# Performance work log

Measured on AMD Instinct MI355X. Metric: run time of the kernel, lower is better.

## Reference

```python
import jax, jax.numpy as jnp
import numpy as np
from jax import lax

S = 3000      # number of stocks (and number of targets)
F = 6         # raw features
N = 128       # hidden size
L = 40        # lookback length
L_MAX = 10    # max lag
K = 5         # topk leaders


def setup_inputs() -> dict:
    key = jax.random.key(0)
    ks = jax.random.split(key, 16)
    sc = 1.0 / np.sqrt(N)
    u = lambda k, shp, s=sc: jax.random.uniform(k, shp, jnp.float32, -s, s)
    return {
        "X_scaled": jax.random.normal(ks[0], (1, S, L, F), jnp.float32),
        "X_raw": jax.random.normal(ks[1], (1, S, L, F), jnp.float32),
        "target_idx": jax.random.randint(ks[2], (S,), 0, S, jnp.int32),
        "lstm_Wih": u(ks[3], (4 * N, F)),
        "lstm_Whh": u(ks[4], (4 * N, N)),
        "lstm_bih": u(ks[5], (4 * N,)),
        "lstm_bhh": u(ks[6], (4 * N,)),
        "ln_g": jnp.ones((N,), jnp.float32),
        "ln_b": jnp.zeros((N,), jnp.float32),
        "WQ": u(ks[7], (N, N)),
        "WK": u(ks[8], (N, N)),
        "log_temp": jnp.asarray(np.log(N ** 0.25), jnp.float32),
        "lag_bias": jnp.zeros((L_MAX,), jnp.float32),
        "W1": u(ks[9], (64, 2 * F), 1.0 / np.sqrt(2 * F)),
        "b1": jnp.zeros((64,), jnp.float32),
        "W2": u(ks[10], (32, 64), 1.0 / 8.0),
        "b2": jnp.zeros((32,), jnp.float32),
        "W3": u(ks[11], (1, 32), 1.0 / np.sqrt(32)),
        "b3": jnp.zeros((1,), jnp.float32),
    }


def _lstm(x, Wih, Whh, bih, bhh):
    # x: [BS, L, F] -> hidden sequence [BS, L, N]; torch gate order i,f,g,o
    BS = x.shape[0]
    h0 = jnp.zeros((BS, N), x.dtype)
    bias = bih + bhh

    def step(carry, xt):
        h, c = carry
        g = xt @ Wih.T + h @ Whh.T + bias
        i, f, gg, o = jnp.split(g, 4, axis=-1)
        c = jax.nn.sigmoid(f) * c + jax.nn.sigmoid(i) * jnp.tanh(gg)
        h = jax.nn.sigmoid(o) * jnp.tanh(c)
        return (h, c), h

    _, hs = lax.scan(step, (h0, h0), jnp.swapaxes(x, 0, 1))
    return jnp.swapaxes(hs, 0, 1)


def _ln(x, g, b):
    m = x.mean(-1, keepdims=True)
    v = ((x - m) ** 2).mean(-1, keepdims=True)
    return (x - m) / jnp.sqrt(v + 1e-5) * g + b


def _l2norm(x):
    return x / jnp.clip(jnp.linalg.norm(x, axis=-1, keepdims=True), 1e-12)


def reference(X_scaled, X_raw, target_idx, lstm_Wih, lstm_Whh, lstm_bih,
              lstm_bhh, ln_g, ln_b, WQ, WK, log_temp, lag_bias,
              W1, b1, W2, b2, W3, b3):
    # TemporalEncoder: LSTM over B*S sequences + LayerNorm (B=1)
    H = _ln(_lstm(X_scaled.reshape(S, L, F), lstm_Wih, lstm_Whh,
                  lstm_bih, lstm_bhh), ln_g, ln_b)          # [S, L, N]
    X = X_raw[0]                                            # [S, L, F]

    q = _l2norm(H[target_idx, -1] @ WQ.T)                   # [T, N]
    Hk = _l2norm(H[:, L - L_MAX:] @ WK.T)                   # [S, l_max, N]
    temp = jnp.clip(jnp.exp(log_temp), 0.1, N ** 0.5)

    attn = jnp.einsum('tn,sln->tsl', q, Hk) / temp + lag_bias  # [T, S, l_max]
    self_mask = jnp.arange(S)[None, :] == target_idx[:, None]  # [T, S]
    attn = jnp.where(self_mask[:, :, None], -jnp.inf, attn)

    vals, idx = lax.top_k(attn.reshape(-1, S * L_MAX), K)   # [T, K]
    leader = idx // L_MAX
    lag_j = idx % L_MAX
    lag_pos = jnp.clip(L - 1 - (L_MAX - lag_j), 0, L - 1)

    z = X[leader, lag_pos]                                  # [T, K, F]
    w = jax.nn.softmax(vals, axis=1)
    z_agg = (w[..., None] * z).sum(1)                       # [T, F]
    feat = jnp.concatenate([z_agg, z[:, 0]], axis=-1)       # [T, 2F]

    h1 = jax.nn.relu(feat @ W1.T + b1)
    h2 = jax.nn.relu(h1 @ W2.T + b2)
    return (h2 @ W3.T + b3).squeeze(-1)                     # [T]
```

## Files before the change

kernel.cpp:

```cpp
#include <hip/hip_runtime.h>
#include <math.h>

#define S_N 3000
#define NCOLS 30000
#define SCHUNK 8
#define KTILES 938
#define TPC 118
#define PST 17

typedef __bf16 v8bf __attribute__((ext_vector_type(8)));
typedef float v16f __attribute__((ext_vector_type(16)));
typedef float v4f __attribute__((ext_vector_type(4)));

__device__ __forceinline__ float sigm(float x) { return 1.0f / (1.0f + expf(-x)); }

__device__ __forceinline__ bool bet(float av, int ai, float bv, int bi) {
  return (av > bv) || (av == bv && ai < bi);
}

template <int M>
__device__ __forceinline__ void insS(float (&v)[M], int (&ix)[M], float nv, int ni) {
  if (!(nv > v[M - 1])) return;
  bool b[M];
#pragma unroll
  for (int q = 0; q < M; q++) b[q] = nv > v[q];
#pragma unroll
  for (int q = M - 1; q > 0; q--) {
    v[q]  = b[q] ? (b[q - 1] ? v[q - 1] : nv) : v[q];
    ix[q] = b[q] ? (b[q - 1] ? ix[q - 1] : ni) : ix[q];
  }
  if (b[0]) { v[0] = nv; ix[0] = ni; }
}

template <int M>
__device__ __forceinline__ void insF(float (&v)[M], int (&ix)[M], float nv, int ni) {
  if (!bet(nv, ni, v[M - 1], ix[M - 1])) return;
  bool b[M];
#pragma unroll
  for (int q = 0; q < M; q++) b[q] = bet(nv, ni, v[q], ix[q]);
#pragma unroll
  for (int q = M - 1; q > 0; q--) {
    v[q]  = b[q] ? (b[q - 1] ? v[q - 1] : nv) : v[q];
    ix[q] = b[q] ? (b[q - 1] ? ix[q - 1] : ni) : ix[q];
  }
  if (b[0]) { v[0] = nv; ix[0] = ni; }
}

__device__ __forceinline__ unsigned short f2bf_rne(float f) {
  unsigned int u = __float_as_uint(f);
  unsigned int r = (u + 0x7fffu + ((u >> 16) & 1u)) >> 16;
  return (unsigned short)r;
}
__device__ __forceinline__ float bf2f(unsigned short h) {
  return __uint_as_float(((unsigned int)h) << 16);
}

__global__ __launch_bounds__(256) void cvt_wll(
    const float* __restrict__ Whh, unsigned short* __restrict__ Wllf)
{
  int idx = blockIdx.x * 256 + threadIdx.x;
  if (idx >= 128 * 512) return;
  int f = idx >> 9;
  int lane = (idx >> 3) & 63;
  int j = idx & 7;
  int w = f >> 3, tau = (f >> 1) & 3, s = f & 1;
  int kh = w >> 3, g8 = w & 7;
  int gate = g8 * 64 + tau * 16 + (lane & 15);
  int k = kh * 64 + s * 32 + (lane >> 4) * 8 + j;
  float x = Whh[gate * 128 + k];
  unsigned short hi = f2bf_rne(x);
  float r1 = x - bf2f(hi);
  unsigned short lo = f2bf_rne(r1);
  float r2 = r1 - bf2f(lo);
  Wllf[idx] = f2bf_rne(r2);
}

__global__ __launch_bounds__(1024, 4) void lstm_kernel(
    const float* __restrict__ Xs, const float* __restrict__ Wih,
    const float* __restrict__ Whh, const float* __restrict__ bih,
    const float* __restrict__ bhh, const unsigned short* __restrict__ Wllf,
    float* __restrict__ H10)
{
  __shared__ float P[2 * 512 * PST];
  __shared__ __align__(16) __bf16 Asp[3][4][65][8];
  __shared__ float Xb[12 * 240];
  __shared__ float2 WB2[14][128];

  const int tid = threadIdx.x;
  const int s0 = blockIdx.x * 12;
  const int lane = tid & 63;
  const int wv = tid >> 6;
  const int kh = wv >> 3;
  const int g8 = wv & 7;
  const int l15 = lane & 15, lq = lane >> 4;

  for (int i = tid; i < 12 * 240; i += 1024) Xb[i] = Xs[(size_t)s0 * 240 + i];
  for (int i = tid; i < 3 * 4 * 65 * 8; i += 1024)
    ((unsigned short*)Asp)[i] = 0;
  for (int i = tid; i < 14 * 128; i += 1024) {
    int q = i >> 7, n = i & 127;
    float vv[2];
#pragma unroll
    for (int e = 0; e < 2; e++) {
      int r = 2 * q + e;
      if (r < 24) {
        int gate = n + (r / 6) * 128;
        vv[e] = Wih[gate * 6 + r % 6];
      } else {
        int gate = n + (r - 24) * 128;
        vv[e] = bih[gate] + bhh[gate];
      }
    }
    WB2[q][n] = make_float2(vv[0], vv[1]);
  }

  v8bf whi[4][2], wlo[4][2];
#pragma unroll
  for (int tau = 0; tau < 4; tau++)
#pragma unroll
    for (int s = 0; s < 2; s++) {
      int gate = g8 * 64 + tau * 16 + l15;
      int k0 = kh * 64 + s * 32 + lq * 8;
      const float* wp = Whh + gate * 128 + k0;
      v8bf h8, l8;
#pragma unroll
      for (int j = 0; j < 8; j++) {
        float x = wp[j];
        __bf16 bh_ = (__bf16)x;
        float r1 = x - (float)bh_;
        __bf16 bl_ = (__bf16)r1;
        h8[j] = bh_;
        l8[j] = bl_;
      }
      whi[tau][s] = h8;
      wlo[tau][s] = l8;
    }

  const unsigned short* wllbase = Wllf + (size_t)(wv * 8) * 512 + lane * 8;

  float c0 = 0.0f, c1 = 0.0f;
  const int p2n = tid & 127;
  const int p2m = tid >> 7;
  const int swl = lane ^ (((lane >> 4) & 3) << 2);

  __syncthreads();

#pragma unroll 1
  for (int t = 0; t < 40; t++) {
    v8bf ah[2], al[2], a3[2];
#pragma unroll
    for (int s = 0; s < 2; s++) {
      int ks = kh * 2 + s;
      ah[s] = *(const v8bf*)&Asp[0][ks][swl][0];
      al[s] = *(const v8bf*)&Asp[1][ks][swl][0];
      a3[s] = *(const v8bf*)&Asp[2][ks][swl][0];
    }
#pragma unroll
    for (int tau = 0; tau < 4; tau++) {
      v4f acc = {0.0f, 0.0f, 0.0f, 0.0f};
#pragma unroll
      for (int s = 0; s < 2; s++) {
        v8bf wll = *(const v8bf*)(wllbase + (tau * 2 + s) * 512);
        acc = __builtin_amdgcn_mfma_f32_16x16x32_bf16(ah[s], whi[tau][s], acc, 0, 0, 0);
        acc = __builtin_amdgcn_mfma_f32_16x16x32_bf16(ah[s], wlo[tau][s], acc, 0, 0, 0);
        acc = __builtin_amdgcn_mfma_f32_16x16x32_bf16(al[s], whi[tau][s], acc, 0, 0, 0);
        acc = __builtin_amdgcn_mfma_f32_16x16x32_bf16(al[s], wlo[tau][s], acc, 0, 0, 0);
        acc = __builtin_amdgcn_mfma_f32_16x16x32_bf16(ah[s], wll, acc, 0, 0, 0);
        acc = __builtin_amdgcn_mfma_f32_16x16x32_bf16(a3[s], whi[tau][s], acc, 0, 0, 0);
      }
      if (lq < 3) {
        int gate = g8 * 64 + tau * 16 + l15;
        float* pp = P + kh * (512 * PST) + gate * PST + lq * 4;
#pragma unroll
        for (int reg = 0; reg < 4; reg++) pp[reg] = acc[reg];
      }
    }
    __syncthreads();

#pragma unroll
    for (int task = 0; task < 2; task++) {
      if (task == 1 && tid >= 512) break;
      const int m = task == 0 ? p2m : 8 + p2m;
      const int n = p2n;
      const float* xm = Xb + m * 240 + t * 6;
      float xv[6];
#pragma unroll
      for (int f = 0; f < 6; f++) xv[f] = xm[f];
      float g4[4];
#pragma unroll
      for (int g = 0; g < 4; g++) {
        float2 w01 = WB2[3 * g][n];
        float2 w23 = WB2[3 * g + 1][n];
        float2 w45 = WB2[3 * g + 2][n];
        float2 bb = WB2[12 + (g >> 1)][n];
        float a = (g & 1) ? bb.y : bb.x;
        a = fmaf(w01.x, xv[0], a);
        a = fmaf(w01.y, xv[1], a);
        a = fmaf(w23.x, xv[2], a);
        a = fmaf(w23.y, xv[3], a);
        a = fmaf(w45.x, xv[4], a);
        a = fmaf(w45.y, xv[5], a);
        int gate = n + g * 128;
        a += P[gate * PST + m] + P[512 * PST + gate * PST + m];
        g4[g] = a;
      }
      float& c = task == 0 ? c0 : c1;
      c = sigm(g4[1]) * c + sigm(g4[0]) * tanhf(g4[2]);
      float h = sigm(g4[3]) * tanhf(c);
      if (t >= 30) H10[((size_t)(s0 + m) * 10 + (t - 30)) * 128 + n] = h;
      __bf16 hh = (__bf16)h;
      float r1 = h - (float)hh;
      __bf16 hl = (__bf16)r1;
      float r2 = r1 - (float)hl;
      __bf16 h3 = (__bf16)r2;
      unsigned a01 = (unsigned)__builtin_bit_cast(unsigned short, hh) |
                     ((unsigned)__builtin_bit_cast(unsigned short, hl) << 16);
      unsigned a2 = (unsigned)__builtin_bit_cast(unsigned short, h3);
      unsigned b01 = (unsigned)__shfl_xor((int)a01, 1);
      unsigned b2 = (unsigned)__shfl_xor((int)a2, 1);
      if (!(lane & 1)) {
        int g = (n >> 3) & 3;
        int ks = n >> 5;
        int row = (m + 16 * g) ^ (g << 2);
        int j0 = n & 7;
        unsigned w0 = (a01 & 0xffffu) | (b01 << 16);
        unsigned w1 = (a01 >> 16) | (b01 & 0xffff0000u);
        unsigned w2 = a2 | (b2 << 16);
        *(unsigned*)&Asp[0][ks][row][j0] = w0;
        *(unsigned*)&Asp[1][ks][row][j0] = w1;
        *(unsigned*)&Asp[2][ks][row][j0] = w2;
      }
    }
    __syncthreads();
  }
}

__global__ __launch_bounds__(256) void proj_kernel(
    const float* __restrict__ In, int inOff, int inStride, int nr,
    const float* __restrict__ W, const float* __restrict__ lng,
    const float* __restrict__ lnb, float* __restrict__ Out,
    unsigned short* __restrict__ OutHi, unsigned short* __restrict__ OutLo)
{
  __shared__ float A_s[16 * 128];
  const int tid = threadIdx.x;
  const int r0 = blockIdx.x * 16;

  for (int i = tid; i < 16 * 32; i += 256) {
    int row = i >> 5, c = i & 31;
    int gr = r0 + row;
    float4 v = make_float4(0.f, 0.f, 0.f, 0.f);
    if (gr < nr)
      v = *(const float4*)(In + (size_t)inOff + (size_t)gr * inStride + c * 4);
    *(float4*)(A_s + row * 128 + c * 4) = v;
  }
  __syncthreads();

  {
    const int wvv = tid >> 6, lane = tid & 63;
    const float g0 = lng[lane], g1 = lng[lane + 64];
    const float bb0 = lnb[lane], bb1 = lnb[lane + 64];
#pragma unroll
    for (int p = 0; p < 4; p++) {
      float* hr = A_s + (wvv * 4 + p) * 128;
      float x0 = hr[lane], x1 = hr[lane + 64];
      float s = x0 + x1;
      for (int off = 32; off > 0; off >>= 1) s += __shfl_xor(s, off);
      float mean = s * (1.0f / 128.0f);
      float d0 = x0 - mean, d1 = x1 - mean;
      float v = d0 * d0 + d1 * d1;
      for (int off = 32; off > 0; off >>= 1) v += __shfl_xor(v, off);
      float rstd = 1.0f / sqrtf(v * (1.0f / 128.0f) + 1e-5f);
      hr[lane] = d0 * rstd * g0 + bb0;
      hr[lane + 64] = d1 * rstd * g1 + bb1;
    }
  }
  __syncthreads();

  const int j = tid & 127, rh = tid >> 7;
  const float* wrow = W + j * 128;
  float acc[8] = {0, 0, 0, 0, 0, 0, 0, 0};
  for (int kc = 0; kc < 32; kc++) {
    float4 wv4 = *(const float4*)(wrow + kc * 4);
#pragma unroll
    for (int i = 0; i < 8; i++) {
      float4 a4 = *(const float4*)(A_s + (rh * 8 + i) * 128 + kc * 4);
      acc[i] = fmaf(wv4.x, a4.x, acc[i]);
      acc[i] = fmaf(wv4.y, a4.y, acc[i]);
      acc[i] = fmaf(wv4.z, a4.z, acc[i]);
      acc[i] = fmaf(wv4.w, a4.w, acc[i]);
    }
  }
  __syncthreads();
#pragma unroll
  for (int i = 0; i < 8; i++) A_s[(rh * 8 + i) * 128 + j] = acc[i];
  __syncthreads();

  const int r = tid >> 4, qq = tid & 15;
  float ss = 0.0f;
#pragma unroll
  for (int i = 0; i < 8; i++) {
    float u = A_s[r * 128 + qq + i * 16];
    ss += u * u;
  }
  for (int off = 8; off > 0; off >>= 1) ss += __shfl_xor(ss, off);
  float scale = 1.0f / fmaxf(sqrtf(ss), 1e-12f);
  int gr = r0 + r;
  if (gr < nr) {
#pragma unroll
    for (int i = 0; i < 8; i++) {
      float val = A_s[r * 128 + qq + i * 16] * scale;
      int col = qq + i * 16;
      Out[(size_t)gr * 128 + col] = val;
      if (OutHi) {
        unsigned short h = f2bf_rne(val);
        unsigned short l = f2bf_rne(val - bf2f(h));
        OutHi[(size_t)gr * 128 + col] = h;
        OutLo[(size_t)gr * 128 + col] = l;
      }
    }
  }
}

__global__ __launch_bounds__(256) void cvt_blockK(
    const float* __restrict__ Kn, unsigned short* __restrict__ hi,
    unsigned short* __restrict__ lo)
{
  const int tile = blockIdx.x;
  const int tid = threadIdx.x;
#pragma unroll
  for (int jj = 0; jj < 4; jj++) {
    int i = tid + jj * 256;
    int r = i >> 5;
    int c0 = (i & 31) * 4;
    int row = tile * 32 + r;
    if (row >= NCOLS) continue;
    float4 f = *(const float4*)(Kn + (size_t)row * 128 + c0);
    ushort4 h, l;
    h.x = f2bf_rne(f.x); l.x = f2bf_rne(f.x - bf2f(h.x));
    h.y = f2bf_rne(f.y); l.y = f2bf_rne(f.y - bf2f(h.y));
    h.z = f2bf_rne(f.z); l.z = f2bf_rne(f.z - bf2f(h.z));
    h.w = f2bf_rne(f.w); l.w = f2bf_rne(f.w - bf2f(h.w));
    int s = c0 >> 4, half = (c0 >> 3) & 1, e = c0 & 7;
    size_t idx = (size_t)tile * 4096 + s * 512 + half * 256 + r * 8 + e;
    *(ushort4*)(hi + idx) = h;
    *(ushort4*)(lo + idx) = l;
  }
}

__global__ __launch_bounds__(256, 3) void score_mfma(
    const unsigned short* __restrict__ Qh, const unsigned short* __restrict__ Ql,
    const unsigned short* __restrict__ Kh, const unsigned short* __restrict__ Kl,
    const int* __restrict__ tix, const float* __restrict__ log_temp,
    const float* __restrict__ lag_bias, float* __restrict__ part)
{
  __shared__ float lagS2[42];
  __shared__ float M[256 * 16];
  const int tid = threadIdx.x;
  const int wv = tid >> 6, lane = tid & 63;
  const int half = lane >> 5, tcol = lane & 31;

  const int lid = blockIdx.y * 94 + blockIdx.x;
  const int chunk = lid & 7;
  const int T0 = (lid >> 3) * 32;
  const int tstart = chunk * TPC;
  const int tend = (tstart + TPC < KTILES) ? tstart + TPC : KTILES;

  for (int i = tid; i < 42; i += 256) lagS2[i] = lag_bias[i % 10];

  const int tgt = T0 + tcol;
  const int tgtc = tgt < S_N ? tgt : S_N - 1;
  const int myTix = tix[tgtc];
  const int selfLo = myTix * 10;
  const float invtemp =
      1.0f / fminf(fmaxf(expf(log_temp[0]), 0.1f), 11.313708499f);

  v8bf bh[8], bl[8];
  {
    const size_t qo = (size_t)myTix * 128 + half * 8;
#pragma unroll
    for (int s = 0; s < 8; s++) {
      bh[s] = *(const v8bf*)(Qh + qo + s * 16);
      bl[s] = *(const v8bf*)(Ql + qo + s * 16);
    }
  }
#pragma unroll
  for (int s = 0; s < 8; s++) {
    asm volatile("" : "+v"(bh[s]), "+v"(bl[s]));
  }

  float tv[8]; int ti[8];
#pragma unroll
  for (int q = 0; q < 8; q++) { tv[q] = -3e38f; ti[q] = 0x7fffffff; }

  __syncthreads();

  for (int it = 0; it < 30; it++) {
    const int tile = tstart + it * 4 + wv;
    const int tilec = tile < KTILES ? tile : KTILES - 1;
    const size_t ao = (size_t)tilec * 4096 + half * 256 + tcol * 8;

    v16f acc0, acc1;
#pragma unroll
    for (int q = 0; q < 16; q++) { acc0[q] = 0.0f; acc1[q] = 0.0f; }

#pragma unroll
    for (int s = 0; s < 8; s++) {
      v8bf ah = *(const v8bf*)(Kh + ao + s * 512);
      v8bf al = *(const v8bf*)(Kl + ao + s * 512);
      acc0 = __builtin_amdgcn_mfma_f32_32x32x16_bf16(ah, bh[s], acc0, 0, 0, 0);
      acc1 = __builtin_amdgcn_mfma_f32_32x32x16_bf16(ah, bl[s], acc1, 0, 0, 0);
      acc1 = __builtin_amdgcn_mfma_f32_32x32x16_bf16(al, bh[s], acc1, 0, 0, 0);
    }

    const int cb = tile * 32;
    const int m0 = cb % 10;
    const bool act = tile < tend;
#pragma unroll
    for (int reg = 0; reg < 16; reg++) {
      const int row = (reg & 3) + 8 * (reg >> 2) + 4 * half;
      const int col = cb + row;
      float vsc = fmaf(acc0[reg] + acc1[reg], invtemp, lagS2[m0 + row]);
      if (act && col < NCOLS && (unsigned)(col - selfLo) >= 10u)
        insS<8>(tv, ti, vsc, col);
    }
  }

  {
    float* my = M + tid * 16;
#pragma unroll
    for (int q = 0; q < 8; q++) {
      my[2 * q] = tv[q];
      my[2 * q + 1] = __int_as_float(ti[q]);
    }
  }
  __syncthreads();
  if (tid < 32 && T0 + tid < S_N) {
    float v[8]; int ix[8];
#pragma unroll
    for (int q = 0; q < 8; q++) { v[q] = -3e38f; ix[q] = 0x7fffffff; }
    for (int w = 0; w < 8; w++) {
      const float* src = M + (w * 32 + tid) * 16;
#pragma unroll
      for (int q = 0; q < 8; q++)
        insF<8>(v, ix, src[2 * q], __float_as_int(src[2 * q + 1]));
    }
    float* dst = part + ((size_t)(T0 + tid) * SCHUNK + chunk) * 16;
#pragma unroll
    for (int q = 0; q < 8; q++) {
      dst[2 * q] = v[q];
      dst[2 * q + 1] = __int_as_float(ix[q]);
    }
  }
}

__global__ __launch_bounds__(256) void final_kernel(
    const float* __restrict__ part, const float* __restrict__ Qn,
    const float* __restrict__ Kn, const int* __restrict__ tix,
    const float* __restrict__ log_temp, const float* __restrict__ lag_bias,
    const float* __restrict__ Xraw,
    const float* __restrict__ W1, const float* __restrict__ b1,
    const float* __restrict__ W2, const float* __restrict__ b2,
    const float* __restrict__ W3, const float* __restrict__ b3,
    float* __restrict__ out)
{
  __shared__ float W1s[64 * 12];
  __shared__ float W2s[32 * 64];
  __shared__ float b1s[64];
  __shared__ float b2s[32];
  __shared__ float W3s[32];
  const int tid = threadIdx.x;
  for (int i = tid; i < 768; i += 256) W1s[i] = W1[i];
  for (int i = tid; i < 2048; i += 256) W2s[i] = W2[i];
  if (tid < 64) b1s[tid] = b1[tid];
  if (tid < 32) { b2s[tid] = b2[tid]; W3s[tid] = W3[tid]; }
  __syncthreads();

  int t = blockIdx.x * 256 + tid;
  if (t >= S_N) return;

  float av[8]; int ai[8];
#pragma unroll
  for (int q = 0; q < 8; q++) { av[q] = -3e38f; ai[q] = 0x7fffffff; }
  const float* pp = part + (size_t)t * (SCHUNK * 16);
  for (int c = 0; c < SCHUNK * 8; c++)
    insF<8>(av, ai, pp[2 * c], __float_as_int(pp[2 * c + 1]));

  const float invtemp =
      1.0f / fminf(fmaxf(expf(log_temp[0]), 0.1f), 11.313708499f);
  const float* q = Qn + (size_t)tix[t] * 128;
  const float* kr[8];
#pragma unroll
  for (int j = 0; j < 8; j++) kr[j] = Kn + (size_t)ai[j] * 128;
  float d[8] = {0, 0, 0, 0, 0, 0, 0, 0};
  for (int kc = 0; kc < 32; kc++) {
    float4 q4 = ((const float4*)q)[kc];
#pragma unroll
    for (int j = 0; j < 8; j++) {
      float4 k4 = ((const float4*)kr[j])[kc];
      d[j] = fmaf(q4.x, k4.x, d[j]);
      d[j] = fmaf(q4.y, k4.y, d[j]);
      d[j] = fmaf(q4.z, k4.z, d[j]);
      d[j] = fmaf(q4.w, k4.w, d[j]);
    }
  }

  float v[5]; int ix[5];
#pragma unroll
  for (int qq = 0; qq < 5; qq++) { v[qq] = -3e38f; ix[qq] = 0x7fffffff; }
#pragma unroll
  for (int j = 0; j < 8; j++) {
    int c = ai[j];
    int s = c / 10;
    int lag = c - 10 * s;
    float ev = d[j] * invtemp + lag_bias[lag];
    insF<5>(v, ix, ev, c);
  }

  float e1 = expf(v[1] - v[0]), e2 = expf(v[2] - v[0]),
        e3 = expf(v[3] - v[0]), e4 = expf(v[4] - v[0]);
  float rs = 1.0f / (1.0f + e1 + e2 + e3 + e4);
  float w_[5] = {rs, e1 * rs, e2 * rs, e3 * rs, e4 * rs};

  float feat[12];
#pragma unroll
  for (int f = 0; f < 12; f++) feat[f] = 0.0f;
#pragma unroll
  for (int qq = 0; qq < 5; qq++) {
    int iq = ix[qq];
    int s = iq / 10;
    int l = iq - 10 * s;
    int pos = 29 + l;
    const float* zp = Xraw + (size_t)s * 240 + pos * 6;
#pragma unroll
    for (int f = 0; f < 6; f++) {
      float z = zp[f];
      feat[f] += w_[qq] * z;
      if (qq == 0) feat[6 + f] = z;
    }
  }

  float h1[64];
#pragma unroll 4
  for (int o = 0; o < 64; o++) {
    float acc = b1s[o];
    const float* wr = W1s + o * 12;
#pragma unroll
    for (int f = 0; f < 12; f++) acc = fmaf(wr[f], feat[f], acc);
    h1[o] = fmaxf(acc, 0.0f);
  }
  float rr = b3[0];
#pragma unroll 2
  for (int o = 0; o < 32; o++) {
    float acc = b2s[o];
    const float* wr = W2s + o * 64;
#pragma unroll 8
    for (int k = 0; k < 64; k++) acc = fmaf(wr[k], h1[k], acc);
    rr = fmaf(W3s[o], fmaxf(acc, 0.0f), rr);
  }
  out[t] = rr;
}

extern "C" void kernel_launch(void* const* d_in, const int* in_sizes, int n_in,
                              void* d_out, int out_size, void* d_ws,
                              size_t ws_size, hipStream_t stream) {
  const float* Xs   = (const float*)d_in[0];
  const float* Xraw = (const float*)d_in[1];
  const int*   tix  = (const int*)d_in[2];
  const float* Wih  = (const float*)d_in[3];
  const float* Whh  = (const float*)d_in[4];
  const float* bih  = (const float*)d_in[5];
  const float* bhh  = (const float*)d_in[6];
  const float* ln_g = (const float*)d_in[7];
  const float* ln_b = (const float*)d_in[8];
  const float* WQ   = (const float*)d_in[9];
  const float* WK   = (const float*)d_in[10];
  const float* log_temp = (const float*)d_in[11];
  const float* lag_bias = (const float*)d_in[12];
  const float* W1 = (const float*)d_in[13];
  const float* b1 = (const float*)d_in[14];
  const float* W2 = (const float*)d_in[15];
  const float* b2 = (const float*)d_in[16];
  const float* W3 = (const float*)d_in[17];
  const float* b3 = (const float*)d_in[18];
  float* outp = (float*)d_out;

  float* ws = (float*)d_ws;
  float* H10 = ws;
  unsigned short* Khi = (unsigned short*)ws;
  unsigned short* Klo = (unsigned short*)(ws + 1922000);
  float* Kn  = ws + 3850000;
  float* Qn  = ws + 7690000;
  unsigned short* Qhi = (unsigned short*)(ws + 8074000);
  unsigned short* Qlo = (unsigned short*)(ws + 8266000);
  float* part = ws + 8458000;
  unsigned short* Wllf = (unsigned short*)(ws + 9226000);

  cvt_wll<<<256, 256, 0, stream>>>(Whh, Wllf);
  lstm_kernel<<<250, 1024, 0, stream>>>(Xs, Wih, Whh, bih, bhh, Wllf, H10);
  proj_kernel<<<1875, 256, 0, stream>>>(H10, 0, 128, 30000, WK, ln_g, ln_b,
                                        Kn, nullptr, nullptr);
  proj_kernel<<<188, 256, 0, stream>>>(H10, 9 * 128, 1280, 3000, WQ, ln_g,
                                       ln_b, Qn, Qhi, Qlo);
  cvt_blockK<<<KTILES, 256, 0, stream>>>(Kn, Khi, Klo);
  {
    dim3 grid(94, SCHUNK);
    score_mfma<<<grid, 256, 0, stream>>>(Qhi, Qlo, Khi, Klo, tix, log_temp,
                                         lag_bias, part);
  }
  final_kernel<<<12, 256, 0, stream>>>(part, Qn, Kn, tix, log_temp, lag_bias,
                                       Xraw, W1, b1, W2, b2, W3, b3, outp);
}
```

Baseline: 687.1 us.

## Merge K/Q projection launches and simplify LSTM hidden-state LDS staging

The K and Q projection kernels are combined into one launch, with the block index choosing which problem each block handles. This removes one kernel launch and lets the two projections share the GPU. Inside the LSTM step, the lane-pair shuffle and packed 32-bit LDS stores are replaced with direct 16-bit bf16 stores, using a new row-rotation swizzle that the MFMA operand reads match. The input weights and bias are also loaded from shared memory into registers before the gate FMAs. The narrower stores may raise LDS store count or cause bank conflicts in the sequential recurrence loop.

Result: no change. 674.1 us (-1.9%).

```diff
diff --git a/kernel.cpp b/kernel.cpp
--- a/kernel.cpp
+++ b/kernel.cpp
@@ -141,7 +141,7 @@
   float c0 = 0.0f, c1 = 0.0f;
   const int p2n = tid & 127;
   const int p2m = tid >> 7;
-  const int swl = lane ^ (((lane >> 4) & 3) << 2);
+  const int rdrow = (lane & 48) | ((lane + 2 * (lane >> 4)) & 15);
 
   __syncthreads();
 
@@ -151,9 +151,9 @@
 #pragma unroll
     for (int s = 0; s < 2; s++) {
       int ks = kh * 2 + s;
-      ah[s] = *(const v8bf*)&Asp[0][ks][swl][0];
-      al[s] = *(const v8bf*)&Asp[1][ks][swl][0];
-      a3[s] = *(const v8bf*)&Asp[2][ks][swl][0];
+      ah[s] = *(const v8bf*)&Asp[0][ks][rdrow][0];
+      al[s] = *(const v8bf*)&Asp[1][ks][rdrow][0];
+      a3[s] = *(const v8bf*)&Asp[2][ks][rdrow][0];
     }
 #pragma unroll
     for (int tau = 0; tau < 4; tau++) {
@@ -182,6 +182,13 @@
       if (task == 1 && tid >= 512) break;
       const int m = task == 0 ? p2m : 8 + p2m;
       const int n = p2n;
+      float wb[28];
+#pragma unroll
+      for (int q = 0; q < 14; q++) {
+        float2 v = WB2[q][n];
+        wb[2 * q] = v.x;
+        wb[2 * q + 1] = v.y;
+      }
       const float* xm = Xb + m * 240 + t * 6;
       float xv[6];
 #pragma unroll
@@ -189,17 +196,9 @@
       float g4[4];
 #pragma unroll
       for (int g = 0; g < 4; g++) {
-        float2 w01 = WB2[3 * g][n];
-        float2 w23 = WB2[3 * g + 1][n];
-        float2 w45 = WB2[3 * g + 2][n];
-        float2 bb = WB2[12 + (g >> 1)][n];
-        float a = (g & 1) ? bb.y : bb.x;
-        a = fmaf(w01.x, xv[0], a);
-        a = fmaf(w01.y, xv[1], a);
-        a = fmaf(w23.x, xv[2], a);
-        a = fmaf(w23.y, xv[3], a);
-        a = fmaf(w45.x, xv[4], a);
-        a = fmaf(w45.y, xv[5], a);
+        float a = wb[24 + g];
+#pragma unroll
+        for (int f = 0; f < 6; f++) a = fmaf(wb[g * 6 + f], xv[f], a);
         int gate = n + g * 128;
         a += P[gate * PST + m] + P[512 * PST + gate * PST + m];
         g4[g] = a;
@@ -213,37 +212,37 @@
       __bf16 hl = (__bf16)r1;
       float r2 = r1 - (float)hl;
       __bf16 h3 = (__bf16)r2;
-      unsigned a01 = (unsigned)__builtin_bit_cast(unsigned short, hh) |
-                     ((unsigned)__builtin_bit_cast(unsigned short, hl) << 16);
-      unsigned a2 = (unsigned)__builtin_bit_cast(unsigned short, h3);
-      unsigned b01 = (unsigned)__shfl_xor((int)a01, 1);
-      unsigned b2 = (unsigned)__shfl_xor((int)a2, 1);
-      if (!(lane & 1)) {
-        int g = (n >> 3) & 3;
-        int ks = n >> 5;
-        int row = (m + 16 * g) ^ (g << 2);
-        int j0 = n & 7;
-        unsigned w0 = (a01 & 0xffffu) | (b01 << 16);
-        unsigned w1 = (a01 >> 16) | (b01 & 0xffff0000u);
-        unsigned w2 = a2 | (b2 << 16);
-        *(unsigned*)&Asp[0][ks][row][j0] = w0;
-        *(unsigned*)&Asp[1][ks][row][j0] = w1;
-        *(unsigned*)&Asp[2][ks][row][j0] = w2;
-      }
+      int g = (n >> 3) & 3;
+      int ks = n >> 5;
+      int j = n & 7;
+      int row = 16 * g + ((m + 2 * g) & 15);
+      Asp[0][ks][row][j] = hh;
+      Asp[1][ks][row][j] = hl;
+      Asp[2][ks][row][j] = h3;
     }
     __syncthreads();
   }
 }
 
 __global__ __launch_bounds__(256) void proj_kernel(
-    const float* __restrict__ In, int inOff, int inStride, int nr,
-    const float* __restrict__ W, const float* __restrict__ lng,
-    const float* __restrict__ lnb, float* __restrict__ Out,
-    unsigned short* __restrict__ OutHi, unsigned short* __restrict__ OutLo)
+    const float* __restrict__ In, const float* __restrict__ WK,
+    const float* __restrict__ WQ, const float* __restrict__ lng,
+    const float* __restrict__ lnb, float* __restrict__ Kn,
+    float* __restrict__ Qn, unsigned short* __restrict__ Qhi,
+    unsigned short* __restrict__ Qlo)
 {
   __shared__ float A_s[16 * 128];
   const int tid = threadIdx.x;
-  const int r0 = blockIdx.x * 16;
+  const int bk = blockIdx.x;
+  const bool isQ = bk >= 1875;
+  const int inOff = isQ ? 9 * 128 : 0;
+  const int inStride = isQ ? 1280 : 128;
+  const int nr = isQ ? 3000 : 30000;
+  const float* W = isQ ? WQ : WK;
+  float* Out = isQ ? Qn : Kn;
+  unsigned short* OutHi = isQ ? Qhi : nullptr;
+  unsigned short* OutLo = isQ ? Qlo : nullptr;
+  const int r0 = (isQ ? bk - 1875 : bk) * 16;
 
   for (int i = tid; i < 16 * 32; i += 256) {
     int row = i >> 5, c = i & 31;
@@ -597,10 +596,8 @@
 
   cvt_wll<<<256, 256, 0, stream>>>(Whh, Wllf);
   lstm_kernel<<<250, 1024, 0, stream>>>(Xs, Wih, Whh, bih, bhh, Wllf, H10);
-  proj_kernel<<<1875, 256, 0, stream>>>(H10, 0, 128, 30000, WK, ln_g, ln_b,
-                                        Kn, nullptr, nullptr);
-  proj_kernel<<<188, 256, 0, stream>>>(H10, 9 * 128, 1280, 3000, WQ, ln_g,
-                                       ln_b, Qn, Qhi, Qlo);
+  proj_kernel<<<2063, 256, 0, stream>>>(H10, WK, WQ, ln_g, ln_b, Kn, Qn,
+                                        Qhi, Qlo);
   cvt_blockK<<<KTILES, 256, 0, stream>>>(Kn, Khi, Klo);
   {
     dim3 grid(94, SCHUNK);
```
